# Optimization experiments

Hardware: AMD Instinct MI355X
Metric: run time of the kernel (lower is better)

Reference implementation:

```python
import jax, jax.numpy as jnp
import numpy as np

NB, NA, NC, NH, NW = 64, 3, 13, 76, 76
NL = 12                     # num_labels per ground-truth row
NET_W = NET_H = 608.0       # net_width / net_height
MAX_T, NVALID = 50, 20      # GT slots per image / number of valid GTs
ANCHORS = np.array([[0.70, 1.18], [1.26, 2.10], [2.64, 4.20]], dtype=np.float32)
BETA = 2.8 / 100.0          # huber beta
EPS = 1e-12
IGNORE_THRESH = 0.5


def iou_cxcywh(b1, b2):
    # boxes [..., 4] in (cx, cy, w, h); matches multi_bbox_ious(x1y1x2y2=False)
    x1, y1, w1, h1 = b1[..., 0], b1[..., 1], b1[..., 2], b1[..., 3]
    x2, y2, w2, h2 = b2[..., 0], b2[..., 1], b2[..., 2], b2[..., 3]
    cw = jnp.minimum(x1 + 0.5 * w1, x2 + 0.5 * w2) - jnp.maximum(x1 - 0.5 * w1, x2 - 0.5 * w2)
    ch = jnp.minimum(y1 + 0.5 * h1, y2 + 0.5 * h2) - jnp.maximum(y1 - 0.5 * h1, y2 - 0.5 * h2)
    inter = jnp.where((cw > 0) & (ch > 0), cw * ch, 0.0)
    return inter / (w1 * h1 + w2 * h2 - inter)


def _bce(p, t):
    # elementwise binary cross entropy with safe logs (torch clamps log, same effect)
    return -(t * jnp.log(jnp.clip(p, EPS, 1.0)) + (1.0 - t) * jnp.log(jnp.clip(1.0 - p, EPS, 1.0)))


def setup_inputs() -> dict:
    key = jax.random.key(0)
    k1, k2, k3, k4, k5 = jax.random.split(key, 5)
    output = jax.random.normal(k1, (NB, NA * (NL + NC), NH, NW), dtype=jnp.float32)
    cls_id = jax.random.randint(k2, (NB, MAX_T), 0, NC).astype(jnp.float32)
    xy = jax.random.uniform(k3, (NB, MAX_T, 2), minval=0.05, maxval=0.95)
    extra = jax.random.uniform(k4, (NB, MAX_T, 7), minval=-0.5, maxval=0.5)
    wh = jax.random.uniform(k5, (NB, MAX_T, 2), minval=0.05, maxval=0.30)
    tbox = jnp.concatenate([cls_id[..., None], xy, extra, wh], axis=-1)  # (NB, 50, 12)
    vmask = (jnp.arange(MAX_T) < NVALID)[None, :, None].astype(jnp.float32)
    target = (tbox * vmask).reshape(NB, MAX_T * NL)  # rows after NVALID are all-zero (break)
    return {"output": output, "target": target, "anchors": jnp.asarray(ANCHORS)}


def _yolo_loss(output, target, anchors):
    target = jax.lax.stop_gradient(target)  # torch: target.detach()
    nB, nA, nC, nH, nW = NB, NA, NC, NH, NW
    nAnchors, nPixels = nA * nH * nW, nH * nW
    cad = nB * nAnchors

    out5 = output.reshape(nB, nA, NL + nC, nH, nW)
    coord = out5[:, :, : NL - 1].reshape(nB * nA, NL - 1, nPixels)
    coord = coord.transpose(1, 0, 2).reshape(NL - 1, cad)          # (11, cad), flat order b,a,h,w
    coord = jnp.concatenate([jax.nn.sigmoid(coord[:2]), coord[2:]], axis=0)
    conf = jax.nn.sigmoid(out5[:, :, NL - 1].reshape(cad))
    cls_logits = out5[:, :, NL:].reshape(nB * nA, nC, nPixels).transpose(0, 2, 1).reshape(cad, nC)

    grid_x = jnp.broadcast_to(jnp.arange(nW, dtype=jnp.float32), (nB * nA, nH, nW)).reshape(cad)
    grid_y = jnp.broadcast_to(jnp.arange(nH, dtype=jnp.float32)[:, None], (nB * nA, nH, nW)).reshape(cad)
    anchor_w = jnp.broadcast_to(anchors[None, :, 0, None], (nB, nA, nPixels)).reshape(cad)
    anchor_h = jnp.broadcast_to(anchors[None, :, 1, None], (nB, nA, nPixels)).reshape(cad)
    pb = jnp.concatenate([
        (coord[0] + grid_x)[None], (coord[1] + grid_y)[None],
        coord[2:9],
        (jnp.exp(coord[9]) * anchor_w)[None], (jnp.exp(coord[10]) * anchor_h)[None],
    ], axis=0)                                                     # (11, cad)
    pred_boxes = jax.lax.stop_gradient(pb.T)                       # detached, as in torch

    # ---- build_targets, vectorized over batch and GT boxes ----
    tbox = target.reshape(nB, MAX_T, NL)
    # emulate the data-dependent `break` at first row with x == 0
    valid = jnp.cumprod((tbox[:, :, 1] > 0).astype(jnp.int32), axis=1).astype(bool)  # (nB,50)
    gx, gy = tbox[:, :, 1] * nW, tbox[:, :, 2] * nH
    gw, gh = tbox[:, :, 10] * NET_W, tbox[:, :, 11] * NET_H

    box_cols = jnp.array([0, 1, 9, 10])
    pbb = pred_boxes.reshape(nB, nAnchors, NL - 1)[:, :, box_cols]  # (nB, nAnchors, 4)
    gtb = jnp.stack([gx, gy, gw, gh], axis=-1)                      # (nB, 50, 4)
    ious_all = iou_cxcywh(pbb[:, None], gtb[:, :, None])            # (nB, 50, nAnchors)
    cur_ious = jnp.where(valid[:, :, None], ious_all, 0.0).max(axis=1)
    noobj = jnp.where(cur_ious > IGNORE_THRESH, 0.0, 1.0).reshape(cad)

    # best anchor by wh IoU at origin
    aw, ah = anchors[:, 0], anchors[:, 1]
    inter = jnp.minimum(gw[..., None], aw) * jnp.minimum(gh[..., None], ah)
    best_n = jnp.argmax(inter / (gw[..., None] * gh[..., None] + aw * ah - inter), axis=-1)  # (nB,50)

    gi = jnp.clip(jnp.floor(gx).astype(jnp.int32), 0, nW - 1)
    gj = jnp.clip(jnp.floor(gy).astype(jnp.int32), 0, nH - 1)
    flat = jnp.arange(nB)[:, None] * nAnchors + best_n * nPixels + gj * nW + gi  # (nB,50)
    pred_sel = pred_boxes[flat.reshape(-1)][:, box_cols].reshape(nB, MAX_T, 4)
    iou_t = iou_cxcywh(gtb, pred_sel)                                # (nB,50)
    idx = jnp.where(valid, flat, cad).reshape(-1)                    # invalid GTs -> dummy slot cad

    aw_b, ah_b = aw[best_n], ah[best_n]
    sgw = jnp.where(valid, gw, 1.0)
    sgh = jnp.where(valid, gh, 1.0)
    vals = jnp.stack([gx - gi.astype(jnp.float32), gy - gj.astype(jnp.float32),
                      tbox[:, :, 3], tbox[:, :, 4], tbox[:, :, 5], tbox[:, :, 6],
                      tbox[:, :, 7], tbox[:, :, 8], tbox[:, :, 9],
                      jnp.log(sgw / aw_b), jnp.log(sgh / ah_b)], axis=-1)  # (nB,50,11)

    obj = jnp.zeros(cad + 1).at[idx].set(1.0)[:cad]
    noobj = jnp.concatenate([noobj, jnp.zeros(1)]).at[idx].set(0.0)[:cad]
    tcoord = jnp.zeros((cad + 1, NL - 1)).at[idx].set(vals.reshape(-1, NL - 1))[:cad].T  # (11,cad)
    tconf = jnp.zeros(cad + 1).at[idx].set(iou_t.reshape(-1))[:cad]   # rescore == 1
    cls_t = tbox[:, :, 0].astype(jnp.int32).reshape(-1)
    tcls = jnp.zeros((cad + 1, nC)).at[idx, cls_t].set(1.0)[:cad]

    # ---- losses: masked sums are equivalent to torch boolean-index-then-sum ----
    m = obj  # (cad,) float {0,1}
    loss_coord = (_bce(coord[0:2], tcoord[0:2]) * m).sum() / nB \
               + (((coord[9:11] - tcoord[9:11]) ** 2) * m).sum() / nB

    diff = (coord[2:5] - tcoord[2:5]) * m                             # (3, cad)
    dis = jnp.sqrt((diff ** 2).sum(axis=1))                           # per-channel L2, as in huber_loss
    in_w = (dis <= BETA).astype(jnp.float32)
    loss_trans = ((0.5 * diff ** 2 / BETA).sum(axis=1) * in_w
                  + (jnp.abs(diff).sum(axis=1) - BETA / 2) * (1.0 - in_w)).sum() / nB

    rot = coord[5:9]
    rot_n = rot / jnp.maximum(jnp.sqrt((rot ** 2).sum(axis=0, keepdims=True)), 1e-12)  # F.normalize dim=0
    loss_rot = (jnp.abs(rot_n - tcoord[5:9]) * m).sum() / nB

    conf_mask = obj + noobj
    loss_conf = _bce(conf * conf_mask, tconf * conf_mask).sum() / nB

    x = cls_logits
    bce_cls = jnp.maximum(x, 0.0) - x * tcls + jnp.log1p(jnp.exp(-jnp.abs(x)))  # BCEWithLogits
    loss_cls = (bce_cls * m[:, None]).sum() / nB

    return loss_coord + loss_trans + loss_rot + loss_conf + loss_cls


def reference(output, target, anchors):
    return _yolo_loss(output, target, anchors)
```

## Files before the change

kernel.cpp:

```cpp
#include <hip/hip_runtime.h>
#include <math.h>

#define NBATCH 64
#define NANCH_PER 3
#define NCLS 13
#define NH 76
#define NW 76
#define NPIX (NH*NW)
#define NG4 (NPIX/4)
#define MAXT 50
#define NLC 12
#define NCH (NLC + NCLS)
#define BETA_C 0.028f
#define EPS_C 1e-12f
#define NET_WH 608.0f
#define SUBB 6
#define NBLK (NBATCH*NANCH_PER*SUBB)
#define LOGEPS 27.6310211159285f

struct TRec {
  float x1, x2, y1, y2;
  float area;
  int   flat;
  float iou;
  int   cls;
  float vals[11];
  float pad;
};

__device__ __forceinline__ float sigmoidf_(float x) { return 1.0f / (1.0f + __expf(-x)); }

__device__ __forceinline__ float bcef_(float p, float t) {
  float lp = __logf(fminf(fmaxf(p, EPS_C), 1.0f));
  float lq = __logf(fminf(fmaxf(1.0f - p, EPS_C), 1.0f));
  return -(t * lp + (1.0f - t) * lq);
}

__global__ void yolo_prep(const float* __restrict__ outp,
                          const float* __restrict__ target,
                          const float* __restrict__ anchors,
                          TRec* __restrict__ recs,
                          float4* __restrict__ boundsA,
                          float* __restrict__ areaA,
                          int* __restrict__ flatA,
                          int* __restrict__ clsA,
                          int* __restrict__ nvalid,
                          float* __restrict__ minarr)
{
  int b = blockIdx.x;
  int t = threadIdx.x;
  const float* tb = target + b * (MAXT * NLC) + t * NLC;
  float v1 = (t < MAXT) ? tb[1] : 0.0f;
  unsigned long long vm = __ballot(v1 > 0.0f);
  bool valid = false;
  float marea = 1e30f;
  if (t < MAXT) {
    valid = ((~vm) & ((2ULL << t) - 1ULL)) == 0ULL;

    float gx = tb[1] * (float)NW, gy = tb[2] * (float)NH;
    float gw = tb[10] * NET_WH,   gh = tb[11] * NET_WH;

    int bn = 0; float best = -1e30f;
    for (int k = 0; k < NANCH_PER; ++k) {
      float aw = anchors[2*k], ah = anchors[2*k+1];
      float inter = fminf(gw, aw) * fminf(gh, ah);
      float r = inter / (gw * gh + aw * ah - inter);
      if (r > best) { best = r; bn = k; }
    }
    float aw = anchors[2*bn], ah = anchors[2*bn+1];

    int gi = min(max((int)floorf(gx), 0), NW - 1);
    int gj = min(max((int)floorf(gy), 0), NH - 1);
    int pixq = gj * NW + gi;
    int flat = bn * NPIX + pixq;

    const float* cb = outp + ((size_t)(b * NANCH_PER + bn) * NCH) * NPIX + pixq;
    float px = sigmoidf_(cb[0]) + (float)gi;
    float py = sigmoidf_(cb[NPIX]) + (float)gj;
    float pw = __expf(cb[9 * NPIX]) * aw;
    float ph = __expf(cb[10 * NPIX]) * ah;

    float cw  = fminf(gx + 0.5f*gw, px + 0.5f*pw) - fmaxf(gx - 0.5f*gw, px - 0.5f*pw);
    float chh = fminf(gy + 0.5f*gh, py + 0.5f*ph) - fmaxf(gy - 0.5f*gh, py - 0.5f*ph);
    float inter = (cw > 0.0f && chh > 0.0f) ? cw * chh : 0.0f;
    float iou = inter / (gw * gh + pw * ph - inter);

    TRec r;
    r.x1 = gx - 0.5f * gw; r.x2 = gx + 0.5f * gw;
    r.y1 = gy - 0.5f * gh; r.y2 = gy + 0.5f * gh;
    r.area = gw * gh;
    r.flat = valid ? flat : -1;
    r.iou = iou;
    r.cls = (int)tb[0];
    r.vals[0] = gx - (float)gi;
    r.vals[1] = gy - (float)gj;
    #pragma unroll
    for (int k = 0; k < 7; ++k) r.vals[2 + k] = tb[3 + k];
    float sgw = valid ? gw : 1.0f, sgh = valid ? gh : 1.0f;
    r.vals[9]  = __logf(sgw / aw);
    r.vals[10] = __logf(sgh / ah);
    r.pad = 0.0f;
    recs[b * MAXT + t] = r;
    boundsA[b * MAXT + t] = make_float4(r.x1, r.x2, r.y1, r.y2);
    areaA[b * MAXT + t] = r.area;
    flatA[b * MAXT + t] = r.flat;
    clsA[b * MAXT + t]  = r.cls;
    if (valid) marea = gw * gh;
  }
  unsigned long long vm2 = __ballot(valid);
  #pragma unroll
  for (int off = 32; off > 0; off >>= 1) marea = fminf(marea, __shfl_xor(marea, off, 64));
  if (t == 0) { nvalid[b] = __popcll(vm2); minarr[b] = marea; }
}

__device__ __forceinline__ float elem4(const float4& v, int e) {
  return e == 0 ? v.x : (e == 1 ? v.y : (e == 2 ? v.z : v.w));
}

__global__ __launch_bounds__(256) void yolo_loss(
    const float* __restrict__ outp,
    const TRec* __restrict__ recs,
    const float4* __restrict__ boundsA,
    const float* __restrict__ areaA,
    const int* __restrict__ flatA,
    const int* __restrict__ clsA,
    const int* __restrict__ nvalid,
    const float* __restrict__ minarr,
    const float* __restrict__ anchors,
    float* __restrict__ partial)
{
  __shared__ float4 s_b4[MAXT];
  __shared__ float  s_area[MAXT];
  __shared__ int    s_flat[MAXT];
  __shared__ int    s_cls[MAXT];
  __shared__ int    s_nv;
  __shared__ float  s_minarea;
  __shared__ unsigned long long s_mask;
  __shared__ float  wsum[4];

  int blk = blockIdx.x;
  int b   = blk / (NANCH_PER * SUBB);
  int rem = blk % (NANCH_PER * SUBB);
  int a   = rem / SUBB;
  int sb  = rem % SUBB;
  int tid = threadIdx.x;

  if (tid < MAXT) {
    s_b4[tid]   = boundsA[b * MAXT + tid];
    s_area[tid] = areaA[b * MAXT + tid];
    s_flat[tid] = flatA[b * MAXT + tid];
    s_cls[tid]  = clsA[b * MAXT + tid];
  }
  if (tid == 0) { s_nv = nvalid[b]; s_minarea = minarr[b]; }
  __syncthreads();

  if (tid < 64) {
    int t = tid;
    bool in = (t < s_nv);
    int f = in ? s_flat[t] : -1;
    int lo = a * NPIX + sb * 1024;
    int hi = a * NPIX + min((sb + 1) * 1024, NPIX);
    unsigned long long mm = __ballot(in && f >= lo && f < hi);
    if (t == 0) s_mask = mm;
  }
  __syncthreads();

  float aw = anchors[2*a], ah = anchors[2*a+1];
  float logthr = __logf(s_minarea / (2.0f * aw * ah));

  const float* plane = outp + ((size_t)(b * NANCH_PER + a) * NCH) * NPIX;
  const float4* tw4p = (const float4*)(plane + 9  * NPIX);
  const float4* th4p = (const float4*)(plane + 10 * NPIX);
  const float4* tc4p = (const float4*)(plane + 11 * NPIX);

  float local = 0.0f;
  int g = sb * 256 + tid;
  if (g < NG4) {
    float4 tw4 = tw4p[g];
    float4 th4 = th4p[g];
    float4 tc4 = tc4p[g];
    unsigned long long mm0 = s_mask;
    #pragma unroll
    for (int e = 0; e < 4; ++e) {
      float tw = elem4(tw4, e), th = elem4(th4, e), tc = elem4(tc4, e);
      int pix = 4 * g + e;
      int myflat = a * NPIX + pix;

      int match = -1;
      unsigned cmask = 0;
      unsigned long long mm = mm0;
      while (mm) {
        int t = (int)__builtin_ctzll(mm); mm &= mm - 1;
        if (s_flat[t] == myflat) { match = t; cmask |= (1u << s_cls[t]); }
      }

      bool over = false;
      if (match < 0 && tw + th > logthr) {
        int j = pix / NW;
        int i = pix - j * NW;
        float sx = sigmoidf_(plane[pix]), sy = sigmoidf_(plane[NPIX + pix]);
        float pw = __expf(tw) * aw, ph = __expf(th) * ah;
        float parea = pw * ph;
        float px = sx + (float)i, py = sy + (float)j;
        float pxl = px - 0.5f * pw, pxh = px + 0.5f * pw;
        float pyl = py - 0.5f * ph, pyh = py + 0.5f * ph;
        int nv = s_nv;
        for (int t = 0; t < nv; ++t) {
          float4 bb = s_b4[t];
          float cw  = fminf(pxh, bb.y) - fmaxf(pxl, bb.x);
          float chh = fminf(pyh, bb.w) - fmaxf(pyl, bb.z);
          float inter = (cw > 0.0f && chh > 0.0f) ? cw * chh : 0.0f;
          over = over || (3.0f * inter > parea + s_area[t]);
        }
      }

      if (match >= 0) {
        int j = pix / NW;
        int i = pix - j * NW;
        float sx = sigmoidf_(plane[pix]), sy = sigmoidf_(plane[NPIX + pix]);
        float conf = sigmoidf_(tc);
        TRec r = recs[b * MAXT + match];
        local += bcef_(conf, r.iou);
        local += bcef_(sx, r.vals[0]) + bcef_(sy, r.vals[1]);
        float d9 = tw - r.vals[9], d10 = th - r.vals[10];
        local += d9 * d9 + d10 * d10;
        float c2 = plane[2*NPIX+pix], c3 = plane[3*NPIX+pix], c4 = plane[4*NPIX+pix];
        float e2 = c2 - r.vals[2], e3 = c3 - r.vals[3], e4 = c4 - r.vals[4];
        float ss = e2*e2 + e3*e3 + e4*e4;
        float dis = sqrtf(ss);
        if (dis <= BETA_C) local += 0.5f * ss / BETA_C;
        else local += fabsf(e2) + fabsf(e3) + fabsf(e4) - 0.5f * BETA_C;
        float c5 = plane[5*NPIX+pix], c6 = plane[6*NPIX+pix];
        float c7 = plane[7*NPIX+pix], c8 = plane[8*NPIX+pix];
        float rn = fmaxf(sqrtf(c5*c5 + c6*c6 + c7*c7 + c8*c8), 1e-12f);
        local += fabsf(c5/rn - r.vals[5]) + fabsf(c6/rn - r.vals[6])
               + fabsf(c7/rn - r.vals[7]) + fabsf(c8/rn - r.vals[8]);
        #pragma unroll
        for (int c = 0; c < NCLS; ++c) {
          float x = plane[(NLC + c) * NPIX + pix];
          float tt = ((cmask >> c) & 1u) ? 1.0f : 0.0f;
          local += fmaxf(x, 0.0f) - x * tt + __logf(1.0f + __expf(-fabsf(x)));
        }
      } else if (!over) {
        local += fminf(__logf(1.0f + __expf(tc)), LOGEPS);
      }
    }
  }

  #pragma unroll
  for (int off = 32; off > 0; off >>= 1) local += __shfl_down(local, off, 64);
  if ((tid & 63) == 0) wsum[tid >> 6] = local;
  __syncthreads();
  if (tid == 0) partial[blk] = wsum[0] + wsum[1] + wsum[2] + wsum[3];
}

__global__ __launch_bounds__(256) void yolo_final(const float* __restrict__ partial,
                                                  float* __restrict__ out)
{
  __shared__ float w[4];
  float s = 0.0f;
  for (int i = threadIdx.x; i < NBLK; i += 256) s += partial[i];
  #pragma unroll
  for (int off = 32; off > 0; off >>= 1) s += __shfl_down(s, off, 64);
  if ((threadIdx.x & 63) == 0) w[threadIdx.x >> 6] = s;
  __syncthreads();
  if (threadIdx.x == 0) out[0] = (w[0] + w[1] + w[2] + w[3]) * (1.0f / (float)NBATCH);
}

extern "C" void kernel_launch(void* const* d_in, const int* in_sizes, int n_in,
                              void* d_out, int out_size, void* d_ws, size_t ws_size,
                              hipStream_t stream) {
  const float* outp    = (const float*)d_in[0];
  const float* target  = (const float*)d_in[1];
  const float* anchors = (const float*)d_in[2];

  char* ws = (char*)d_ws;
  size_t off = 0;
  TRec*   recs    = (TRec*)  (ws + off); off += (size_t)NBATCH * MAXT * sizeof(TRec);
  float4* boundsA = (float4*)(ws + off); off += (size_t)NBATCH * MAXT * sizeof(float4);
  float*  areaA   = (float*) (ws + off); off += (size_t)NBATCH * MAXT * sizeof(float);
  int*    flatA   = (int*)   (ws + off); off += (size_t)NBATCH * MAXT * sizeof(int);
  int*    clsA    = (int*)   (ws + off); off += (size_t)NBATCH * MAXT * sizeof(int);
  int*    nv      = (int*)   (ws + off); off += 256;
  float*  minarr  = (float*) (ws + off); off += 256;
  float*  partial = (float*) (ws + off);

  yolo_prep<<<NBATCH, 64, 0, stream>>>(outp, target, anchors, recs, boundsA, areaA,
                                       flatA, clsA, nv, minarr);
  yolo_loss<<<NBLK, 256, 0, stream>>>(outp, recs, boundsA, areaA, flatA, clsA,
                                      nv, minarr, anchors, partial);
  yolo_final<<<1, 256, 0, stream>>>(partial, (float*)d_out);
}
```

Before: 158.2 us.

## Fuse prep, loss and final reduction into one kernel with atomic accumulation

```diff
diff --git a/kernel.cpp b/kernel.cpp
--- a/kernel.cpp
+++ b/kernel.cpp
@@ -18,16 +18,6 @@
 #define NBLK (NBATCH*NANCH_PER*SUBB)
 #define LOGEPS 27.6310211159285f
 
-struct TRec {
-  float x1, x2, y1, y2;
-  float area;
-  int   flat;
-  float iou;
-  int   cls;
-  float vals[11];
-  float pad;
-};
-
 __device__ __forceinline__ float sigmoidf_(float x) { return 1.0f / (1.0f + __expf(-x)); }
 
 __device__ __forceinline__ float bcef_(float p, float t) {
@@ -36,105 +26,24 @@
   return -(t * lp + (1.0f - t) * lq);
 }
 
-__global__ void yolo_prep(const float* __restrict__ outp,
-                          const float* __restrict__ target,
-                          const float* __restrict__ anchors,
-                          TRec* __restrict__ recs,
-                          float4* __restrict__ boundsA,
-                          float* __restrict__ areaA,
-                          int* __restrict__ flatA,
-                          int* __restrict__ clsA,
-                          int* __restrict__ nvalid,
-                          float* __restrict__ minarr)
-{
-  int b = blockIdx.x;
-  int t = threadIdx.x;
-  const float* tb = target + b * (MAXT * NLC) + t * NLC;
-  float v1 = (t < MAXT) ? tb[1] : 0.0f;
-  unsigned long long vm = __ballot(v1 > 0.0f);
-  bool valid = false;
-  float marea = 1e30f;
-  if (t < MAXT) {
-    valid = ((~vm) & ((2ULL << t) - 1ULL)) == 0ULL;
-
-    float gx = tb[1] * (float)NW, gy = tb[2] * (float)NH;
-    float gw = tb[10] * NET_WH,   gh = tb[11] * NET_WH;
-
-    int bn = 0; float best = -1e30f;
-    for (int k = 0; k < NANCH_PER; ++k) {
-      float aw = anchors[2*k], ah = anchors[2*k+1];
-      float inter = fminf(gw, aw) * fminf(gh, ah);
-      float r = inter / (gw * gh + aw * ah - inter);
-      if (r > best) { best = r; bn = k; }
-    }
-    float aw = anchors[2*bn], ah = anchors[2*bn+1];
-
-    int gi = min(max((int)floorf(gx), 0), NW - 1);
-    int gj = min(max((int)floorf(gy), 0), NH - 1);
-    int pixq = gj * NW + gi;
-    int flat = bn * NPIX + pixq;
-
-    const float* cb = outp + ((size_t)(b * NANCH_PER + bn) * NCH) * NPIX + pixq;
-    float px = sigmoidf_(cb[0]) + (float)gi;
-    float py = sigmoidf_(cb[NPIX]) + (float)gj;
-    float pw = __expf(cb[9 * NPIX]) * aw;
-    float ph = __expf(cb[10 * NPIX]) * ah;
-
-    float cw  = fminf(gx + 0.5f*gw, px + 0.5f*pw) - fmaxf(gx - 0.5f*gw, px - 0.5f*pw);
-    float chh = fminf(gy + 0.5f*gh, py + 0.5f*ph) - fmaxf(gy - 0.5f*gh, py - 0.5f*ph);
-    float inter = (cw > 0.0f && chh > 0.0f) ? cw * chh : 0.0f;
-    float iou = inter / (gw * gh + pw * ph - inter);
-
-    TRec r;
-    r.x1 = gx - 0.5f * gw; r.x2 = gx + 0.5f * gw;
-    r.y1 = gy - 0.5f * gh; r.y2 = gy + 0.5f * gh;
-    r.area = gw * gh;
-    r.flat = valid ? flat : -1;
-    r.iou = iou;
-    r.cls = (int)tb[0];
-    r.vals[0] = gx - (float)gi;
-    r.vals[1] = gy - (float)gj;
-    #pragma unroll
-    for (int k = 0; k < 7; ++k) r.vals[2 + k] = tb[3 + k];
-    float sgw = valid ? gw : 1.0f, sgh = valid ? gh : 1.0f;
-    r.vals[9]  = __logf(sgw / aw);
-    r.vals[10] = __logf(sgh / ah);
-    r.pad = 0.0f;
-    recs[b * MAXT + t] = r;
-    boundsA[b * MAXT + t] = make_float4(r.x1, r.x2, r.y1, r.y2);
-    areaA[b * MAXT + t] = r.area;
-    flatA[b * MAXT + t] = r.flat;
-    clsA[b * MAXT + t]  = r.cls;
-    if (valid) marea = gw * gh;
-  }
-  unsigned long long vm2 = __ballot(valid);
-  #pragma unroll
-  for (int off = 32; off > 0; off >>= 1) marea = fminf(marea, __shfl_xor(marea, off, 64));
-  if (t == 0) { nvalid[b] = __popcll(vm2); minarr[b] = marea; }
-}
-
 __device__ __forceinline__ float elem4(const float4& v, int e) {
   return e == 0 ? v.x : (e == 1 ? v.y : (e == 2 ? v.z : v.w));
 }
 
-__global__ __launch_bounds__(256) void yolo_loss(
+__global__ __launch_bounds__(256) void yolo_fused(
     const float* __restrict__ outp,
-    const TRec* __restrict__ recs,
-    const float4* __restrict__ boundsA,
-    const float* __restrict__ areaA,
-    const int* __restrict__ flatA,
-    const int* __restrict__ clsA,
-    const int* __restrict__ nvalid,
-    const float* __restrict__ minarr,
+    const float* __restrict__ target,
     const float* __restrict__ anchors,
-    float* __restrict__ partial)
+    float* __restrict__ out)
 {
   __shared__ float4 s_b4[MAXT];
   __shared__ float  s_area[MAXT];
   __shared__ int    s_flat[MAXT];
   __shared__ int    s_cls[MAXT];
+  __shared__ float  s_iou[MAXT];
+  __shared__ float  s_vals[MAXT][11];
   __shared__ int    s_nv;
-  __shared__ float  s_minarea;
+  __shared__ float  s_logthr;
   __shared__ unsigned long long s_mask;
   __shared__ float  wsum[4];
 
@@ -145,28 +54,74 @@
   int sb  = rem % SUBB;
   int tid = threadIdx.x;
 
-  if (tid < MAXT) {
-    s_b4[tid]   = boundsA[b * MAXT + tid];
-    s_area[tid] = areaA[b * MAXT + tid];
-    s_flat[tid] = flatA[b * MAXT + tid];
-    s_cls[tid]  = clsA[b * MAXT + tid];
-  }
-  if (tid == 0) { s_nv = nvalid[b]; s_minarea = minarr[b]; }
-  __syncthreads();
+  float awb = anchors[2*a], ahb = anchors[2*a+1];
 
   if (tid < 64) {
     int t = tid;
-    bool in = (t < s_nv);
-    int f = in ? s_flat[t] : -1;
+    const float* tb = target + b * (MAXT * NLC) + t * NLC;
+    float v1 = (t < MAXT) ? tb[1] : 0.0f;
+    unsigned long long vm = __ballot(v1 > 0.0f);
+    bool valid = false;
+    float marea = 1e30f;
+    int flat = -1;
+    if (t < MAXT) {
+      valid = ((~vm) & ((2ULL << t) - 1ULL)) == 0ULL;
+
+      float gx = tb[1] * (float)NW, gy = tb[2] * (float)NH;
+      float gw = tb[10] * NET_WH,   gh = tb[11] * NET_WH;
+
+      int bn = 0; float best = -1e30f;
+      for (int k = 0; k < NANCH_PER; ++k) {
+        float aw = anchors[2*k], ah = anchors[2*k+1];
+        float inter = fminf(gw, aw) * fminf(gh, ah);
+        float r = inter / (gw * gh + aw * ah - inter);
+        if (r > best) { best = r; bn = k; }
+      }
+      float aw = anchors[2*bn], ah = anchors[2*bn+1];
+
+      int gi = min(max((int)floorf(gx), 0), NW - 1);
+      int gj = min(max((int)floorf(gy), 0), NH - 1);
+      int pixq = gj * NW + gi;
+      flat = valid ? (bn * NPIX + pixq) : -1;
+
+      const float* cb = outp + ((size_t)(b * NANCH_PER + bn) * NCH) * NPIX + pixq;
+      float px = sigmoidf_(cb[0]) + (float)gi;
+      float py = sigmoidf_(cb[NPIX]) + (float)gj;
+      float pw = __expf(cb[9 * NPIX]) * aw;
+      float ph = __expf(cb[10 * NPIX]) * ah;
+
+      float cw  = fminf(gx + 0.5f*gw, px + 0.5f*pw) - fmaxf(gx - 0.5f*gw, px - 0.5f*pw);
+      float chh = fminf(gy + 0.5f*gh, py + 0.5f*ph) - fmaxf(gy - 0.5f*gh, py - 0.5f*ph);
+      float inter = (cw > 0.0f && chh > 0.0f) ? cw * chh : 0.0f;
+      float iou = inter / (gw * gh + pw * ph - inter);
+
+      s_b4[t]   = make_float4(gx - 0.5f*gw, gx + 0.5f*gw, gy - 0.5f*gh, gy + 0.5f*gh);
+      s_area[t] = gw * gh;
+      s_flat[t] = flat;
+      s_cls[t]  = (int)tb[0];
+      s_iou[t]  = iou;
+      s_vals[t][0] = gx - (float)gi;
+      s_vals[t][1] = gy - (float)gj;
+      #pragma unroll
+      for (int k = 0; k < 7; ++k) s_vals[t][2 + k] = tb[3 + k];
+      float sgw = valid ? gw : 1.0f, sgh = valid ? gh : 1.0f;
+      s_vals[t][9]  = __logf(sgw / aw);
+      s_vals[t][10] = __logf(sgh / ah);
+      if (valid) marea = gw * gh;
+    }
+    unsigned long long vm2 = __ballot(valid);
     int lo = a * NPIX + sb * 1024;
     int hi = a * NPIX + min((sb + 1) * 1024, NPIX);
-    unsigned long long mm = __ballot(in && f >= lo && f < hi);
-    if (t == 0) s_mask = mm;
+    unsigned long long mm = __ballot(valid && flat >= lo && flat < hi);
+    #pragma unroll
+    for (int off = 32; off > 0; off >>= 1) marea = fminf(marea, __shfl_xor(marea, off, 64));
+    if (t == 0) {
+      s_nv = __popcll(vm2);
+      s_mask = mm;
+      s_logthr = __logf(marea / (2.0f * awb * ahb));
+    }
   }
   __syncthreads();
-
-  float aw = anchors[2*a], ah = anchors[2*a+1];
-  float logthr = __logf(s_minarea / (2.0f * aw * ah));
 
   const float* plane = outp + ((size_t)(b * NANCH_PER + a) * NCH) * NPIX;
   const float4* tw4p = (const float4*)(plane + 9  * NPIX);
@@ -179,27 +134,34 @@
     float4 tw4 = tw4p[g];
     float4 th4 = th4p[g];
     float4 tc4 = tc4p[g];
-    unsigned long long mm0 = s_mask;
+    float logthr = s_logthr;
+
+    int   mt[4]; unsigned cm[4];
+    #pragma unroll
+    for (int e = 0; e < 4; ++e) { mt[e] = -1; cm[e] = 0; }
+    int base = a * NPIX + 4 * g;
+    unsigned long long mm = s_mask;
+    while (mm) {
+      int t = (int)__builtin_ctzll(mm); mm &= mm - 1;
+      int rel = s_flat[t] - base;
+      int cls = s_cls[t];
+      #pragma unroll
+      for (int e = 0; e < 4; ++e)
+        if (rel == e) { mt[e] = t; cm[e] |= (1u << cls); }
+    }
+
     #pragma unroll
     for (int e = 0; e < 4; ++e) {
       float tw = elem4(tw4, e), th = elem4(th4, e), tc = elem4(tc4, e);
       int pix = 4 * g + e;
-      int myflat = a * NPIX + pix;
-
-      int match = -1;
-      unsigned cmask = 0;
-      unsigned long long mm = mm0;
-      while (mm) {
-        int t = (int)__builtin_ctzll(mm); mm &= mm - 1;
-        if (s_flat[t] == myflat) { match = t; cmask |= (1u << s_cls[t]); }
-      }
+      int match = mt[e];
 
       bool over = false;
       if (match < 0 && tw + th > logthr) {
         int j = pix / NW;
         int i = pix - j * NW;
         float sx = sigmoidf_(plane[pix]), sy = sigmoidf_(plane[NPIX + pix]);
-        float pw = __expf(tw) * aw, ph = __expf(th) * ah;
+        float pw = __expf(tw) * awb, ph = __expf(th) * ahb;
         float parea = pw * ph;
         float px = sx + (float)i, py = sy + (float)j;
         float pxl = px - 0.5f * pw, pxh = px + 0.5f * pw;
@@ -219,13 +181,12 @@
         int i = pix - j * NW;
         float sx = sigmoidf_(plane[pix]), sy = sigmoidf_(plane[NPIX + pix]);
         float conf = sigmoidf_(tc);
-        TRec r = recs[b * MAXT + match];
-        local += bcef_(conf, r.iou);
-        local += bcef_(sx, r.vals[0]) + bcef_(sy, r.vals[1]);
-        float d9 = tw - r.vals[9], d10 = th - r.vals[10];
+        local += bcef_(conf, s_iou[match]);
+        local += bcef_(sx, s_vals[match][0]) + bcef_(sy, s_vals[match][1]);
+        float d9 = tw - s_vals[match][9], d10 = th - s_vals[match][10];
         local += d9 * d9 + d10 * d10;
         float c2 = plane[2*NPIX+pix], c3 = plane[3*NPIX+pix], c4 = plane[4*NPIX+pix];
-        float e2 = c2 - r.vals[2], e3 = c3 - r.vals[3], e4 = c4 - r.vals[4];
+        float e2 = c2 - s_vals[match][2], e3 = c3 - s_vals[match][3], e4 = c4 - s_vals[match][4];
         float ss = e2*e2 + e3*e3 + e4*e4;
         float dis = sqrtf(ss);
         if (dis <= BETA_C) local += 0.5f * ss / BETA_C;
@@ -233,8 +194,9 @@
         float c5 = plane[5*NPIX+pix], c6 = plane[6*NPIX+pix];
         float c7 = plane[7*NPIX+pix], c8 = plane[8*NPIX+pix];
         float rn = fmaxf(sqrtf(c5*c5 + c6*c6 + c7*c7 + c8*c8), 1e-12f);
-        local += fabsf(c5/rn - r.vals[5]) + fabsf(c6/rn - r.vals[6])
-               + fabsf(c7/rn - r.vals[7]) + fabsf(c8/rn - r.vals[8]);
+        local += fabsf(c5/rn - s_vals[match][5]) + fabsf(c6/rn - s_vals[match][6])
+               + fabsf(c7/rn - s_vals[match][7]) + fabsf(c8/rn - s_vals[match][8]);
+        unsigned cmask = cm[e];
         #pragma unroll
         for (int c = 0; c < NCLS; ++c) {
           float x = plane[(NLC + c) * NPIX + pix];
@@ -251,20 +213,8 @@
   for (int off = 32; off > 0; off >>= 1) local += __shfl_down(local, off, 64);
   if ((tid & 63) == 0) wsum[tid >> 6] = local;
   __syncthreads();
-  if (tid == 0) partial[blk] = wsum[0] + wsum[1] + wsum[2] + wsum[3];
-}
-
-__global__ __launch_bounds__(256) void yolo_final(const float* __restrict__ partial,
-                                                  float* __restrict__ out)
-{
-  __shared__ float w[4];
-  float s = 0.0f;
-  for (int i = threadIdx.x; i < NBLK; i += 256) s += partial[i];
-  #pragma unroll
-  for (int off = 32; off > 0; off >>= 1) s += __shfl_down(s, off, 64);
-  if ((threadIdx.x & 63) == 0) w[threadIdx.x >> 6] = s;
-  __syncthreads();
-  if (threadIdx.x == 0) out[0] = (w[0] + w[1] + w[2] + w[3]) * (1.0f / (float)NBATCH);
+  if (tid == 0)
+    atomicAdd(out, (wsum[0] + wsum[1] + wsum[2] + wsum[3]) * (1.0f / (float)NBATCH));
 }
 
 extern "C" void kernel_launch(void* const* d_in, const int* in_sizes, int n_in,
@@ -274,20 +224,6 @@
   const float* target  = (const float*)d_in[1];
   const float* anchors = (const float*)d_in[2];
 
-  char* ws = (char*)d_ws;
-  size_t off = 0;
-  TRec*   recs    = (TRec*)  (ws + off); off += (size_t)NBATCH * MAXT * sizeof(TRec);
-  float4* boundsA = (float4*)(ws + off); off += (size_t)NBATCH * MAXT * sizeof(float4);
-  float*  areaA   = (float*) (ws + off); off += (size_t)NBATCH * MAXT * sizeof(float);
-  int*    flatA   = (int*)   (ws + off); off += (size_t)NBATCH * MAXT * sizeof(int);
-  int*    clsA    = (int*)   (ws + off); off += (size_t)NBATCH * MAXT * sizeof(int);
-  int*    nv      = (int*)   (ws + off); off += 256;
-  float*  minarr  = (float*) (ws + off); off += 256;
-  float*  partial = (float*) (ws + off);
-
-  yolo_prep<<<NBATCH, 64, 0, stream>>>(outp, target, anchors, recs, boundsA, areaA,
-                                       flatA, clsA, nv, minarr);
-  yolo_loss<<<NBLK, 256, 0, stream>>>(outp, recs, boundsA, areaA, flatA, clsA,
-                                      nv, minarr, anchors, partial);
-  yolo_final<<<1, 256, 0, stream>>>(partial, (float*)d_out);
-}
+  hipMemsetAsync(d_out, 0, sizeof(float), stream);
+  yolo_fused<<<NBLK, 256, 0, stream>>>(outp, target, anchors, (float*)d_out);
+}
```

Measured after the change: 162.1 us. 2.5% more time.
